# Kernel tuning notes

Measured on AMD Instinct MI355X. Metric: run time of the kernel, lower is better.

## Reference

```python
import jax, jax.numpy as jnp
import numpy as np

T = 4096        # tokens (batch*seq flattened)
H = 1024        # hidden_size
F = 2816        # intermediate_size
E = 8           # num_experts
TOPK = 2        # num_experts_per_tok


def setup_inputs() -> dict:
    key = jax.random.key(0)
    ks = jax.random.split(key, 5)
    scale_h = 1.0 / np.sqrt(H)
    scale_f = 1.0 / np.sqrt(F)
    return {
        "x": jax.random.normal(ks[0], (T, H), dtype=jnp.float32),
        "w_router": jax.random.normal(ks[1], (H, E), dtype=jnp.float32) * scale_h,
        "w_gate": jax.random.normal(ks[2], (E, H, F), dtype=jnp.float32) * scale_h,
        "w_up": jax.random.normal(ks[3], (E, H, F), dtype=jnp.float32) * scale_h,
        "w_down": jax.random.normal(ks[4], (E, F, H), dtype=jnp.float32) * scale_f,
    }


def reference(x, w_router, w_gate, w_up, w_down):
    # Router: softmax over experts, top-k select, renormalize selected weights.
    router_logits = x @ w_router                      # [T, E]
    probs = jax.nn.softmax(router_logits, axis=-1)    # [T, E]
    top_w, top_i = jax.lax.top_k(probs, TOPK)         # [T, K]
    top_w = top_w / jnp.sum(top_w, axis=-1, keepdims=True)
    # Dense per-token-per-expert combine weights (0 for unselected experts).
    # Equivalent to the one_hot(selected_experts) mask + index_add scatter-combine.
    dense_w = jnp.sum(jax.nn.one_hot(top_i, E, dtype=x.dtype) * top_w[..., None], axis=1)  # [T, E]
    # Expert MLPs (gate/up -> silu*mul -> down), computed for all experts and
    # masked by dense_w (zero weight => zero contribution), matching the
    # gather-GEMM-scatter math exactly.
    g = jnp.einsum('th,ehf->etf', x, w_gate)          # [E, T, F]
    u = jnp.einsum('th,ehf->etf', x, w_up)            # [E, T, F]
    a = jax.nn.silu(g) * u                            # silu_mul
    d = jnp.einsum('etf,efh->eth', a, w_down)         # [E, T, H]
    out = jnp.einsum('eth,te->th', d, dense_w)        # weighted scatter-add combine
    return out
```

## Files before the change

kernel.cpp:

```cpp
#include <hip/hip_runtime.h>
#include <hip/hip_bf16.h>
#include <stdint.h>

#define T_TOK 4096
#define H_DIM 1024
#define F_DIM 2816
#define NE 8
#define NTILE_MAX 72

using bf16x8 = __attribute__((ext_vector_type(8))) short;
using f32x16 = __attribute__((ext_vector_type(16))) float;

__device__ __forceinline__ unsigned short f2bf(float f) {
    union { float f; uint32_t u; } v; v.f = f;
    uint32_t r = v.u + 0x7FFFu + ((v.u >> 16) & 1u);
    return (unsigned short)(r >> 16);
}

__device__ __forceinline__ void gload_lds16(const void* gsrc, void* lds) {
    __builtin_amdgcn_global_load_lds(
        (const __attribute__((address_space(1))) uint32_t*)gsrc,
        (__attribute__((address_space(3))) uint32_t*)lds, 16, 0, 0);
}

__global__ __launch_bounds__(256) void router_kernel(
    const float* __restrict__ x, const float* __restrict__ wr,
    unsigned short* __restrict__ xbf,
    int* __restrict__ top_i, float* __restrict__ top_w)
{
    const int w = threadIdx.x >> 6, l = threadIdx.x & 63;
    const int tok = blockIdx.x * 4 + w;
    const float* xrow = x + (size_t)tok * H_DIM;
    unsigned short* xbrow = xbf + (size_t)tok * H_DIM;
    float acc[NE] = {};
    for (int h = l; h < H_DIM; h += 64) {
        float xv = xrow[h];
        xbrow[h] = f2bf(xv);
#pragma unroll
        for (int e = 0; e < NE; e++) acc[e] += xv * wr[h * NE + e];
    }
#pragma unroll
    for (int e = 0; e < NE; e++) {
        for (int off = 32; off; off >>= 1) acc[e] += __shfl_xor(acc[e], off);
    }
    if (l == 0) {
        int i1 = 0; float b1 = acc[0];
#pragma unroll
        for (int e = 1; e < NE; e++) if (acc[e] > b1) { b1 = acc[e]; i1 = e; }
        int i2 = -1; float b2 = -1e30f;
#pragma unroll
        for (int e = 0; e < NE; e++) if (e != i1 && acc[e] > b2) { b2 = acc[e]; i2 = e; }
        float w1 = 1.0f / (1.0f + __expf(b2 - b1));
        top_i[tok * 2] = i1; top_i[tok * 2 + 1] = i2;
        top_w[tok * 2] = w1; top_w[tok * 2 + 1] = 1.0f - w1;
    }
}

__global__ __launch_bounds__(256) void prefix_scatter_kernel(
    const int* __restrict__ top_i,
    int* __restrict__ offsets, int* __restrict__ wtab,
    int* __restrict__ pair_tok, int* __restrict__ inv_pos)
{
    __shared__ int scnt[NE];
    __shared__ int scur[NE];
    if (threadIdx.x < NE) scnt[threadIdx.x] = 0;
    __syncthreads();
    for (int tok = threadIdx.x; tok < T_TOK; tok += 256) {
        atomicAdd(&scnt[top_i[tok * 2]], 1);
        atomicAdd(&scnt[top_i[tok * 2 + 1]], 1);
    }
    __syncthreads();
    if (threadIdx.x == 0) {
        int s = 0;
        for (int e = 0; e < NE; e++) { offsets[e] = s; scur[e] = s; s += scnt[e]; }
        offsets[NE] = s;
        int idx = 0;
        for (int e = 0; e < NE; e++) {
            int nt = (scnt[e] + 127) >> 7;
            for (int mt = 0; mt < nt && idx < NTILE_MAX; ++mt) wtab[idx++] = (e << 16) | mt;
        }
        while (idx < NTILE_MAX) wtab[idx++] = -1;
    }
    __syncthreads();
    for (int tok = threadIdx.x; tok < T_TOK; tok += 256) {
#pragma unroll
        for (int k = 0; k < 2; k++) {
            int e = top_i[tok * 2 + k];
            int pos = atomicAdd(&scur[e], 1);
            pair_tok[pos] = tok;
            inv_pos[tok * 2 + k] = pos;
        }
    }
}

__device__ __forceinline__ void transpose_tile_v3(
    const float* __restrict__ inp, unsigned short* __restrict__ oute,
    int R, int C, int r0, int c0, int t)
{
    __shared__ uint32_t tile[64][33];
#pragma unroll
    for (int p = 0; p < 4; ++p) {
        int r = p * 16 + (t >> 4);
        float4 v = *(const float4*)&inp[(size_t)(r0 + r) * C + c0 + (t & 15) * 4];
        tile[r][(t & 15) * 2]     = (uint32_t)f2bf(v.x) | ((uint32_t)f2bf(v.y) << 16);
        tile[r][(t & 15) * 2 + 1] = (uint32_t)f2bf(v.z) | ((uint32_t)f2bf(v.w) << 16);
    }
    __syncthreads();
#pragma unroll
    for (int p = 0; p < 2; ++p) {
        int oc = p * 32 + (t >> 3);
        int rb = (t & 7) * 8;
        int cp = oc >> 1, sh = (oc & 1) * 16;
        unsigned short u[8];
#pragma unroll
        for (int i = 0; i < 8; ++i) u[i] = (unsigned short)(tile[rb + i][cp] >> sh);
        uint4 o;
        o.x = (uint32_t)u[0] | ((uint32_t)u[1] << 16);
        o.y = (uint32_t)u[2] | ((uint32_t)u[3] << 16);
        o.z = (uint32_t)u[4] | ((uint32_t)u[5] << 16);
        o.w = (uint32_t)u[6] | ((uint32_t)u[7] << 16);
        *(uint4*)&oute[(size_t)(c0 + oc) * R + r0 + rb] = o;
    }
}

__global__ __launch_bounds__(256) void transpose_cvt_v3(
    const float* __restrict__ in, unsigned short* __restrict__ outp, int R, int C)
{
    const int e = blockIdx.z;
    transpose_tile_v3(in + (size_t)e * R * C, outp + (size_t)e * R * C,
                      R, C, blockIdx.y * 64, blockIdx.x * 64, threadIdx.x);
}

__global__ __launch_bounds__(256) void transpose_cvt_gu3(
    const float* __restrict__ wg, const float* __restrict__ wu,
    unsigned short* __restrict__ wgT, unsigned short* __restrict__ wuT)
{
    const int z = blockIdx.z;
    const int e = z & 7;
    const float* inp = (z < 8 ? wg : wu) + (size_t)e * H_DIM * F_DIM;
    unsigned short* oute = (z < 8 ? wgT : wuT) + (size_t)e * H_DIM * F_DIM;
    transpose_tile_v3(inp, oute, H_DIM, F_DIM,
                      blockIdx.y * 64, blockIdx.x * 64, threadIdx.x);
}

__global__ __launch_bounds__(256, 4) void gemm1_kernel(
    const unsigned short* __restrict__ xbf,
    const unsigned short* __restrict__ wgT,
    const unsigned short* __restrict__ wuT,
    const int* __restrict__ pair_tok, const int* __restrict__ offsets,
    const int* __restrict__ wtab,
    unsigned short* __restrict__ Abuf)
{
    const int wv = wtab[blockIdx.y];
    if (wv < 0) return;
    const int e = wv >> 16;
    const int m0 = (wv & 0xFFFF) * 128;
    const int off = offsets[e], Ne = offsets[e + 1] - off;
    const int bn0 = blockIdx.x * 64;

    __shared__ unsigned short smem[16384];
    unsigned short* sA = smem;
    char* sG = (char*)smem + 16384;
    char* sU = (char*)smem + 24576;

    const int t = threadIdx.x, l = t & 63, w = t >> 6;
    const int l31 = l & 31, h5 = l >> 5;
    const int wm = w >> 1, wn = w & 1;
    const int slr = l >> 3, slc = l & 7;

    const unsigned short* srcA[4];
#pragma unroll
    for (int i = 0; i < 4; ++i) {
        int s = w * 4 + i;
        int r = s * 8 + slr;
        int pr = m0 + r; if (pr > Ne - 1) pr = Ne - 1;
        srcA[i] = xbf + (size_t)pair_tok[off + pr] * H_DIM + (slc ^ (r & 7)) * 8;
    }
    const unsigned short* srcG[2];
    const unsigned short* srcU[2];
#pragma unroll
    for (int i = 0; i < 2; ++i) {
        int s = w * 2 + i;
        int fr = s * 8 + slr;
        srcG[i] = wgT + ((size_t)e * F_DIM + bn0 + fr) * H_DIM + (slc ^ (fr & 7)) * 8;
        srcU[i] = wuT + ((size_t)e * F_DIM + bn0 + fr) * H_DIM + (slc ^ (fr & 7)) * 8;
    }

    int aoff[2][4], goff[4];
#pragma unroll
    for (int mm = 0; mm < 2; ++mm) {
        int row = wm * 64 + mm * 32 + l31;
#pragma unroll
        for (int kk = 0; kk < 4; ++kk)
            aoff[mm][kk] = row * 128 + (((kk * 2 + h5) ^ (row & 7)) * 16);
    }
    {
        int g = wn * 32 + l31;
#pragma unroll
        for (int kk = 0; kk < 4; ++kk)
            goff[kk] = g * 128 + (((kk * 2 + h5) ^ (g & 7)) * 16);
    }

    f32x16 accG[2] = {}, accU[2] = {};

    for (int k0 = 0; k0 < H_DIM; k0 += 64) {
        __syncthreads();
#pragma unroll
        for (int i = 0; i < 4; ++i)
            gload_lds16(srcA[i] + k0, (char*)sA + (w * 4 + i) * 1024);
#pragma unroll
        for (int i = 0; i < 2; ++i) {
            gload_lds16(srcG[i] + k0, sG + (w * 2 + i) * 1024);
            gload_lds16(srcU[i] + k0, sU + (w * 2 + i) * 1024);
        }
        asm volatile("s_waitcnt vmcnt(0)" ::: "memory");
        __syncthreads();

#pragma unroll
        for (int kk = 0; kk < 4; ++kk) {
            bf16x8 a0 = *(const bf16x8*)((const char*)sA + aoff[0][kk]);
            bf16x8 a1 = *(const bf16x8*)((const char*)sA + aoff[1][kk]);
            bf16x8 gf = *(const bf16x8*)(sG + goff[kk]);
            bf16x8 uf = *(const bf16x8*)(sU + goff[kk]);
            __builtin_amdgcn_s_setprio(1);
            accG[0] = __builtin_amdgcn_mfma_f32_32x32x16_bf16(a0, gf, accG[0], 0, 0, 0);
            accG[1] = __builtin_amdgcn_mfma_f32_32x32x16_bf16(a1, gf, accG[1], 0, 0, 0);
            accU[0] = __builtin_amdgcn_mfma_f32_32x32x16_bf16(a0, uf, accU[0], 0, 0, 0);
            accU[1] = __builtin_amdgcn_mfma_f32_32x32x16_bf16(a1, uf, accU[1], 0, 0, 0);
            __builtin_amdgcn_s_setprio(0);
        }
    }

#pragma unroll
    for (int mm = 0; mm < 2; ++mm) {
#pragma unroll
        for (int r = 0; r < 16; ++r) {
            int grow = m0 + wm * 64 + mm * 32 + (r & 3) + 8 * (r >> 2) + 4 * h5;
            if (grow < Ne) {
                size_t p = (size_t)(off + grow);
                float g = accG[mm][r], u = accU[mm][r];
                float a = g / (1.0f + __expf(-g)) * u;
                Abuf[p * F_DIM + bn0 + wn * 32 + l31] = f2bf(a);
            }
        }
    }
}

__global__ __launch_bounds__(256, 4) void gemm2_kernel(
    const unsigned short* __restrict__ Abuf,
    const unsigned short* __restrict__ wdT,
    const int* __restrict__ offsets, const int* __restrict__ wtab,
    unsigned short* __restrict__ dbuf)
{
    const int wv = wtab[blockIdx.y];
    if (wv < 0) return;
    const int e = wv >> 16;
    const int m0 = (wv & 0xFFFF) * 128;
    const int off = offsets[e], Ne = offsets[e + 1] - off;
    const int bn0 = blockIdx.x * 128;

    __shared__ unsigned short smem[16384];
    unsigned short* sA = smem;
    char* sB = (char*)smem + 16384;

    const int t = threadIdx.x, l = t & 63, w = t >> 6;
    const int l31 = l & 31, h5 = l >> 5;
    const int wm = w >> 1, wn = w & 1;
    const int slr = l >> 3, slc = l & 7;

    const unsigned short* srcA[4];
    const unsigned short* srcB[4];
#pragma unroll
    for (int i = 0; i < 4; ++i) {
        int s = w * 4 + i;
        int r = s * 8 + slr;
        int pr = m0 + r; if (pr > Ne - 1) pr = Ne - 1;
        srcA[i] = Abuf + (size_t)(off + pr) * F_DIM + (slc ^ (r & 7)) * 8;
        srcB[i] = wdT + ((size_t)e * H_DIM + bn0 + r) * F_DIM + (slc ^ (r & 7)) * 8;
    }

    int aoff[2][4], boff[2][4];
#pragma unroll
    for (int mm = 0; mm < 2; ++mm) {
        int row = wm * 64 + mm * 32 + l31;
        int brow = wn * 64 + mm * 32 + l31;
#pragma unroll
        for (int kk = 0; kk < 4; ++kk) {
            aoff[mm][kk] = row * 128 + (((kk * 2 + h5) ^ (row & 7)) * 16);
            boff[mm][kk] = brow * 128 + (((kk * 2 + h5) ^ (brow & 7)) * 16);
        }
    }

    f32x16 acc[2][2] = {};

    for (int k0 = 0; k0 < F_DIM; k0 += 64) {
        __syncthreads();
#pragma unroll
        for (int i = 0; i < 4; ++i) {
            gload_lds16(srcA[i] + k0, (char*)sA + (w * 4 + i) * 1024);
            gload_lds16(srcB[i] + k0, sB + (w * 4 + i) * 1024);
        }
        asm volatile("s_waitcnt vmcnt(0)" ::: "memory");
        __syncthreads();

#pragma unroll
        for (int kk = 0; kk < 4; ++kk) {
            bf16x8 a0  = *(const bf16x8*)((const char*)sA + aoff[0][kk]);
            bf16x8 a1  = *(const bf16x8*)((const char*)sA + aoff[1][kk]);
            bf16x8 b0  = *(const bf16x8*)(sB + boff[0][kk]);
            bf16x8 b1  = *(const bf16x8*)(sB + boff[1][kk]);
            __builtin_amdgcn_s_setprio(1);
            acc[0][0] = __builtin_amdgcn_mfma_f32_32x32x16_bf16(a0, b0, acc[0][0], 0, 0, 0);
            acc[0][1] = __builtin_amdgcn_mfma_f32_32x32x16_bf16(a0, b1, acc[0][1], 0, 0, 0);
            acc[1][0] = __builtin_amdgcn_mfma_f32_32x32x16_bf16(a1, b0, acc[1][0], 0, 0, 0);
            acc[1][1] = __builtin_amdgcn_mfma_f32_32x32x16_bf16(a1, b1, acc[1][1], 0, 0, 0);
            __builtin_amdgcn_s_setprio(0);
        }
    }

#pragma unroll
    for (int mm = 0; mm < 2; ++mm) {
#pragma unroll
        for (int r = 0; r < 16; ++r) {
            int grow = m0 + wm * 64 + mm * 32 + (r & 3) + 8 * (r >> 2) + 4 * h5;
            if (grow < Ne) {
                size_t p = (size_t)(off + grow);
#pragma unroll
                for (int nn = 0; nn < 2; ++nn)
                    dbuf[p * H_DIM + bn0 + wn * 64 + nn * 32 + l31] = f2bf(acc[mm][nn][r]);
            }
        }
    }
}

__global__ __launch_bounds__(256) void combine_kernel(
    const unsigned short* __restrict__ dbuf, const int* __restrict__ inv_pos,
    const float* __restrict__ top_w, float* __restrict__ out)
{
    int tok = blockIdx.x;
    int p0 = inv_pos[tok * 2], p1 = inv_pos[tok * 2 + 1];
    float w0 = top_w[tok * 2], w1 = top_w[tok * 2 + 1];
    int c = threadIdx.x * 4;
    ushort4 a = *(const ushort4*)&dbuf[(size_t)p0 * H_DIM + c];
    ushort4 b = *(const ushort4*)&dbuf[(size_t)p1 * H_DIM + c];
    union { uint32_t u; float f; } ca, cb;
    float4 o;
    ca.u = (uint32_t)a.x << 16; cb.u = (uint32_t)b.x << 16; o.x = w0 * ca.f + w1 * cb.f;
    ca.u = (uint32_t)a.y << 16; cb.u = (uint32_t)b.y << 16; o.y = w0 * ca.f + w1 * cb.f;
    ca.u = (uint32_t)a.z << 16; cb.u = (uint32_t)b.z << 16; o.z = w0 * ca.f + w1 * cb.f;
    ca.u = (uint32_t)a.w << 16; cb.u = (uint32_t)b.w << 16; o.w = w0 * ca.f + w1 * cb.f;
    *(float4*)&out[(size_t)tok * H_DIM + c] = o;
}

extern "C" void kernel_launch(void* const* d_in, const int* in_sizes, int n_in,
                              void* d_out, int out_size, void* d_ws, size_t ws_size,
                              hipStream_t stream)
{
    const float* x  = (const float*)d_in[0];
    const float* wr = (const float*)d_in[1];
    const float* wg = (const float*)d_in[2];
    const float* wu = (const float*)d_in[3];
    const float* wd = (const float*)d_in[4];
    float* out = (float*)d_out;

    char* ws = (char*)d_ws;
    const size_t WT = (size_t)NE * F_DIM * H_DIM * 2;
    unsigned short* wgT  = (unsigned short*)(ws);
    unsigned short* wuT  = (unsigned short*)(ws + WT);
    unsigned short* Abuf = (unsigned short*)(ws + 2 * WT);
    unsigned short* xbf  = (unsigned short*)(ws + 3 * WT);
    char* misc = ws + 3 * WT + (size_t)T_TOK * H_DIM * 2;
    int*   pair_tok = (int*)(misc);
    int*   top_i    = (int*)(misc + 32768);
    float* top_w    = (float*)(misc + 65536);
    int*   inv_pos  = (int*)(misc + 98304);
    int*   offsets  = (int*)(misc + 131072);
    int*   wtab     = offsets + 9;
    unsigned short* wdT = wgT;
    unsigned short* dbuf = wuT;

    transpose_cvt_gu3<<<dim3(F_DIM / 64, H_DIM / 64, 16), 256, 0, stream>>>(wg, wu, wgT, wuT);
    router_kernel<<<T_TOK / 4, 256, 0, stream>>>(x, wr, xbf, top_i, top_w);
    prefix_scatter_kernel<<<1, 256, 0, stream>>>(top_i, offsets, wtab, pair_tok, inv_pos);
    gemm1_kernel<<<dim3(F_DIM / 64, NTILE_MAX), 256, 0, stream>>>(xbf, wgT, wuT, pair_tok, offsets, wtab, Abuf);
    transpose_cvt_v3<<<dim3(H_DIM / 64, F_DIM / 64, NE), 256, 0, stream>>>(wd, wdT, F_DIM, H_DIM);
    gemm2_kernel<<<dim3(H_DIM / 128, NTILE_MAX), 256, 0, stream>>>(Abuf, wdT, offsets, wtab, dbuf);
    combine_kernel<<<T_TOK, 256, 0, stream>>>(dbuf, inv_pos, top_w, out);
}
```

Measured before the change: 309.6 us.

## Split-K gemm2 into two halves and switch gemm1 to 16x16x32 MFMA tiles

Result: faster. 292.2 us, median of 2 (-5.6%).

```diff
diff --git a/kernel.cpp b/kernel.cpp
--- a/kernel.cpp
+++ b/kernel.cpp
@@ -6,9 +6,11 @@
 #define H_DIM 1024
 #define F_DIM 2816
 #define NE 8
+#define NPAIR (T_TOK * 2)
 #define NTILE_MAX 72
 
 using bf16x8 = __attribute__((ext_vector_type(8))) short;
+using f32x4  = __attribute__((ext_vector_type(4))) float;
 using f32x16 = __attribute__((ext_vector_type(16))) float;
 
 __device__ __forceinline__ unsigned short f2bf(float f) {
@@ -164,7 +166,7 @@
     char* sU = (char*)smem + 24576;
 
     const int t = threadIdx.x, l = t & 63, w = t >> 6;
-    const int l31 = l & 31, h5 = l >> 5;
+    const int llo = l & 15, lhi = l >> 4;
     const int wm = w >> 1, wn = w & 1;
     const int slr = l >> 3, slc = l & 7;
 
@@ -186,22 +188,23 @@
         srcU[i] = wuT + ((size_t)e * F_DIM + bn0 + fr) * H_DIM + (slc ^ (fr & 7)) * 8;
     }
 
-    int aoff[2][4], goff[4];
-#pragma unroll
-    for (int mm = 0; mm < 2; ++mm) {
-        int row = wm * 64 + mm * 32 + l31;
-#pragma unroll
-        for (int kk = 0; kk < 4; ++kk)
-            aoff[mm][kk] = row * 128 + (((kk * 2 + h5) ^ (row & 7)) * 16);
-    }
-    {
-        int g = wn * 32 + l31;
-#pragma unroll
-        for (int kk = 0; kk < 4; ++kk)
-            goff[kk] = g * 128 + (((kk * 2 + h5) ^ (g & 7)) * 16);
-    }
-
-    f32x16 accG[2] = {}, accU[2] = {};
+    int aoff[4][2], goff[2][2];
+#pragma unroll
+    for (int m = 0; m < 4; ++m) {
+        int row = wm * 64 + m * 16 + llo;
+#pragma unroll
+        for (int kk = 0; kk < 2; ++kk)
+            aoff[m][kk] = row * 128 + (((kk * 4 + lhi) ^ (row & 7)) * 16);
+    }
+#pragma unroll
+    for (int n = 0; n < 2; ++n) {
+        int g = wn * 32 + n * 16 + llo;
+#pragma unroll
+        for (int kk = 0; kk < 2; ++kk)
+            goff[n][kk] = g * 128 + (((kk * 4 + lhi) ^ (g & 7)) * 16);
+    }
+
+    f32x4 accG[4][2] = {}, accU[4][2] = {};
 
     for (int k0 = 0; k0 < H_DIM; k0 += 64) {
         __syncthreads();
@@ -217,30 +220,40 @@
         __syncthreads();
 
 #pragma unroll
-        for (int kk = 0; kk < 4; ++kk) {
-            bf16x8 a0 = *(const bf16x8*)((const char*)sA + aoff[0][kk]);
-            bf16x8 a1 = *(const bf16x8*)((const char*)sA + aoff[1][kk]);
-            bf16x8 gf = *(const bf16x8*)(sG + goff[kk]);
-            bf16x8 uf = *(const bf16x8*)(sU + goff[kk]);
+        for (int kk = 0; kk < 2; ++kk) {
+            bf16x8 af[4], gf[2], uf[2];
+#pragma unroll
+            for (int m = 0; m < 4; ++m) af[m] = *(const bf16x8*)((const char*)sA + aoff[m][kk]);
+#pragma unroll
+            for (int n = 0; n < 2; ++n) {
+                gf[n] = *(const bf16x8*)(sG + goff[n][kk]);
+                uf[n] = *(const bf16x8*)(sU + goff[n][kk]);
+            }
             __builtin_amdgcn_s_setprio(1);
-            accG[0] = __builtin_amdgcn_mfma_f32_32x32x16_bf16(a0, gf, accG[0], 0, 0, 0);
-            accG[1] = __builtin_amdgcn_mfma_f32_32x32x16_bf16(a1, gf, accG[1], 0, 0, 0);
-            accU[0] = __builtin_amdgcn_mfma_f32_32x32x16_bf16(a0, uf, accU[0], 0, 0, 0);
-            accU[1] = __builtin_amdgcn_mfma_f32_32x32x16_bf16(a1, uf, accU[1], 0, 0, 0);
+#pragma unroll
+            for (int m = 0; m < 4; ++m)
+#pragma unroll
+                for (int n = 0; n < 2; ++n) {
+                    accG[m][n] = __builtin_amdgcn_mfma_f32_16x16x32_bf16(af[m], gf[n], accG[m][n], 0, 0, 0);
+                    accU[m][n] = __builtin_amdgcn_mfma_f32_16x16x32_bf16(af[m], uf[n], accU[m][n], 0, 0, 0);
+                }
             __builtin_amdgcn_s_setprio(0);
         }
     }
 
 #pragma unroll
-    for (int mm = 0; mm < 2; ++mm) {
-#pragma unroll
-        for (int r = 0; r < 16; ++r) {
-            int grow = m0 + wm * 64 + mm * 32 + (r & 3) + 8 * (r >> 2) + 4 * h5;
+    for (int m = 0; m < 4; ++m) {
+#pragma unroll
+        for (int r = 0; r < 4; ++r) {
+            int grow = m0 + wm * 64 + m * 16 + lhi * 4 + r;
             if (grow < Ne) {
                 size_t p = (size_t)(off + grow);
-                float g = accG[mm][r], u = accU[mm][r];
-                float a = g / (1.0f + __expf(-g)) * u;
-                Abuf[p * F_DIM + bn0 + wn * 32 + l31] = f2bf(a);
+#pragma unroll
+                for (int n = 0; n < 2; ++n) {
+                    float g = accG[m][n][r], u = accU[m][n][r];
+                    float a = g / (1.0f + __expf(-g)) * u;
+                    Abuf[p * F_DIM + bn0 + wn * 32 + n * 16 + llo] = f2bf(a);
+                }
             }
         }
     }
@@ -258,6 +271,8 @@
     const int m0 = (wv & 0xFFFF) * 128;
     const int off = offsets[e], Ne = offsets[e + 1] - off;
     const int bn0 = blockIdx.x * 128;
+    const int kbase = blockIdx.z * (F_DIM / 2);
+    unsigned short* dout = dbuf + (size_t)blockIdx.z * NPAIR * H_DIM;
 
     __shared__ unsigned short smem[16384];
     unsigned short* sA = smem;
@@ -275,8 +290,8 @@
         int s = w * 4 + i;
         int r = s * 8 + slr;
         int pr = m0 + r; if (pr > Ne - 1) pr = Ne - 1;
-        srcA[i] = Abuf + (size_t)(off + pr) * F_DIM + (slc ^ (r & 7)) * 8;
-        srcB[i] = wdT + ((size_t)e * H_DIM + bn0 + r) * F_DIM + (slc ^ (r & 7)) * 8;
+        srcA[i] = Abuf + (size_t)(off + pr) * F_DIM + kbase + (slc ^ (r & 7)) * 8;
+        srcB[i] = wdT + ((size_t)e * H_DIM + bn0 + r) * F_DIM + kbase + (slc ^ (r & 7)) * 8;
     }
 
     int aoff[2][4], boff[2][4];
@@ -293,7 +308,7 @@
 
     f32x16 acc[2][2] = {};
 
-    for (int k0 = 0; k0 < F_DIM; k0 += 64) {
+    for (int k0 = 0; k0 < F_DIM / 2; k0 += 64) {
         __syncthreads();
 #pragma unroll
         for (int i = 0; i < 4; ++i) {
@@ -327,7 +342,7 @@
                 size_t p = (size_t)(off + grow);
 #pragma unroll
                 for (int nn = 0; nn < 2; ++nn)
-                    dbuf[p * H_DIM + bn0 + wn * 64 + nn * 32 + l31] = f2bf(acc[mm][nn][r]);
+                    dout[p * H_DIM + bn0 + wn * 64 + nn * 32 + l31] = f2bf(acc[mm][nn][r]);
             }
         }
     }
@@ -340,15 +355,22 @@
     int tok = blockIdx.x;
     int p0 = inv_pos[tok * 2], p1 = inv_pos[tok * 2 + 1];
     float w0 = top_w[tok * 2], w1 = top_w[tok * 2 + 1];
+    const unsigned short* d1 = dbuf + (size_t)NPAIR * H_DIM;
     int c = threadIdx.x * 4;
-    ushort4 a = *(const ushort4*)&dbuf[(size_t)p0 * H_DIM + c];
-    ushort4 b = *(const ushort4*)&dbuf[(size_t)p1 * H_DIM + c];
-    union { uint32_t u; float f; } ca, cb;
+    ushort4 a0 = *(const ushort4*)&dbuf[(size_t)p0 * H_DIM + c];
+    ushort4 a1 = *(const ushort4*)&d1[(size_t)p0 * H_DIM + c];
+    ushort4 b0 = *(const ushort4*)&dbuf[(size_t)p1 * H_DIM + c];
+    ushort4 b1 = *(const ushort4*)&d1[(size_t)p1 * H_DIM + c];
+    union { uint32_t u; float f; } va, vb, vc, vd;
     float4 o;
-    ca.u = (uint32_t)a.x << 16; cb.u = (uint32_t)b.x << 16; o.x = w0 * ca.f + w1 * cb.f;
-    ca.u = (uint32_t)a.y << 16; cb.u = (uint32_t)b.y << 16; o.y = w0 * ca.f + w1 * cb.f;
-    ca.u = (uint32_t)a.z << 16; cb.u = (uint32_t)b.z << 16; o.z = w0 * ca.f + w1 * cb.f;
-    ca.u = (uint32_t)a.w << 16; cb.u = (uint32_t)b.w << 16; o.w = w0 * ca.f + w1 * cb.f;
+    va.u = (uint32_t)a0.x << 16; vb.u = (uint32_t)a1.x << 16; vc.u = (uint32_t)b0.x << 16; vd.u = (uint32_t)b1.x << 16;
+    o.x = w0 * (va.f + vb.f) + w1 * (vc.f + vd.f);
+    va.u = (uint32_t)a0.y << 16; vb.u = (uint32_t)a1.y << 16; vc.u = (uint32_t)b0.y << 16; vd.u = (uint32_t)b1.y << 16;
+    o.y = w0 * (va.f + vb.f) + w1 * (vc.f + vd.f);
+    va.u = (uint32_t)a0.z << 16; vb.u = (uint32_t)a1.z << 16; vc.u = (uint32_t)b0.z << 16; vd.u = (uint32_t)b1.z << 16;
+    o.z = w0 * (va.f + vb.f) + w1 * (vc.f + vd.f);
+    va.u = (uint32_t)a0.w << 16; vb.u = (uint32_t)a1.w << 16; vc.u = (uint32_t)b0.w << 16; vd.u = (uint32_t)b1.w << 16;
+    o.w = w0 * (va.f + vb.f) + w1 * (vc.f + vd.f);
     *(float4*)&out[(size_t)tok * H_DIM + c] = o;
 }
 
@@ -384,6 +406,6 @@
     prefix_scatter_kernel<<<1, 256, 0, stream>>>(top_i, offsets, wtab, pair_tok, inv_pos);
     gemm1_kernel<<<dim3(F_DIM / 64, NTILE_MAX), 256, 0, stream>>>(xbf, wgT, wuT, pair_tok, offsets, wtab, Abuf);
     transpose_cvt_v3<<<dim3(H_DIM / 64, F_DIM / 64, NE), 256, 0, stream>>>(wd, wdT, F_DIM, H_DIM);
-    gemm2_kernel<<<dim3(H_DIM / 128, NTILE_MAX), 256, 0, stream>>>(Abuf, wdT, offsets, wtab, dbuf);
+    gemm2_kernel<<<dim3(H_DIM / 128, NTILE_MAX, 2), 256, 0, stream>>>(Abuf, wdT, offsets, wtab, dbuf);
     combine_kernel<<<T_TOK, 256, 0, stream>>>(dbuf, inv_pos, top_w, out);
 }
```
